# Optimization experiments

Hardware: AMD Instinct MI355X
Metric: run time of the kernel (lower is better)

The kernel has to match this reference:

```python
import math
import jax, jax.numpy as jnp
import numpy as np

B, C_IN, H, W = 2, 64, 256, 512
C_OUT, KH, KW = 64, 3, 3
STRIDE, PAD, DIL = 1, 1, 1


def equi_offsets(pano_H, pano_W, kH, kW, dtype=jnp.float32):
    """Geometry-derived per-pixel offsets for equirectangular deform-conv.
    Returns (off_y, off_x), each [K, pano_H, pano_W], K = kH*kW (row-major)."""
    K = kH * kW
    u = jnp.arange(pano_W, dtype=dtype)
    v = jnp.arange(pano_H, dtype=dtype)
    phi = (u - pano_W / 2.0) / pano_W * (2.0 * math.pi)   # longitude per column
    theta = -(v - pano_H / 2.0) / pano_H * math.pi        # latitude per row
    # R_y(phi): [W,3,3]
    cp, sp = jnp.cos(phi), jnp.sin(phi)
    z, o = jnp.zeros_like(cp), jnp.ones_like(cp)
    Ry = jnp.stack([jnp.stack([cp, z, sp], -1),
                    jnp.stack([z, o, z], -1),
                    jnp.stack([-sp, z, cp], -1)], -2)
    # R_x(theta): [H,3,3]
    ct, st = jnp.cos(theta), jnp.sin(theta)
    zh, oh = jnp.zeros_like(ct), jnp.ones_like(ct)
    Rx = jnp.stack([jnp.stack([oh, zh, zh], -1),
                    jnp.stack([zh, ct, -st], -1),
                    jnp.stack([zh, st, ct], -1)], -2)
    ROT = jnp.einsum('wij,hjk->hwik', Ry, Rx)             # [H,W,3,3]
    # Pinhole rays for the kernel window
    fov_w = kW * (2.0 * math.pi / pano_W)
    focal = (kW / 2.0) / math.tan(fov_w / 2.0)
    hg = (jnp.arange(kH, dtype=dtype)[:, None] + 0.5 - kH / 2.0)
    wg = (jnp.arange(kW, dtype=dtype)[None, :] + 0.5 - kW / 2.0)
    hg = jnp.broadcast_to(hg, (kH, kW)).reshape(K)
    wg = jnp.broadcast_to(wg, (kH, kW)).reshape(K)
    rays0 = jnp.stack([wg / focal, hg / focal, jnp.ones(K, dtype)], 0)  # inv_K @ [w,h,1]
    rays0 = rays0 / jnp.linalg.norm(rays0, axis=0, keepdims=True)
    rays = jnp.einsum('hwik,kn->hwin', ROT, rays0)        # [H,W,3,K]
    phi2 = jnp.arctan2(rays[..., 0, :], rays[..., 2, :])
    th2 = jnp.arcsin(jnp.clip(rays[..., 1, :], -1.0, 1.0))
    x = pano_W / (2.0 * math.pi) * phi2 + pano_W / 2.0    # [H,W,K]
    y = pano_H / math.pi * th2 + pano_H / 2.0
    off_x = x - (wg[None, None, :] + u[None, :, None])
    off_y = y - (hg[None, None, :] + v[:, None, None])
    return jnp.transpose(off_y, (2, 0, 1)), jnp.transpose(off_x, (2, 0, 1))


def deform_conv2d(x, weight, bias, off_y, off_x, stride, pad, dil):
    """Deformable conv (groups=1) with zero-padded bilinear sampling.
    x: [B,C,Hi,Wi]; weight: [O,C,kH,kW]; off_y/off_x: [K,Ho,Wo]."""
    Bn, C, Hi, Wi = x.shape
    O, _, kH, kW = weight.shape
    K, Ho, Wo = off_y.shape
    ky = jnp.broadcast_to(jnp.arange(kH)[:, None], (kH, kW)).reshape(K).astype(x.dtype)
    kx = jnp.broadcast_to(jnp.arange(kW)[None, :], (kH, kW)).reshape(K).astype(x.dtype)
    base_y = jnp.arange(Ho, dtype=x.dtype) * stride - pad
    base_x = jnp.arange(Wo, dtype=x.dtype) * stride - pad
    py = base_y[None, :, None] + ky[:, None, None] * dil + off_y   # [K,Ho,Wo]
    px = base_x[None, None, :] + kx[:, None, None] * dil + off_x
    y0f = jnp.floor(py)
    x0f = jnp.floor(px)
    wy1 = py - y0f
    wx1 = px - x0f
    iy0 = y0f.astype(jnp.int32)
    ix0 = x0f.astype(jnp.int32)
    iy1, ix1 = iy0 + 1, ix0 + 1
    xf = x.reshape(Bn, C, Hi * Wi)

    def corner(iy, ix, w):
        valid = (iy >= 0) & (iy < Hi) & (ix >= 0) & (ix < Wi)
        idx = jnp.clip(iy, 0, Hi - 1) * Wi + jnp.clip(ix, 0, Wi - 1)
        g = xf[:, :, idx]                                  # [B,C,K,Ho,Wo]
        return g * (w * valid.astype(x.dtype))[None, None]

    samp = (corner(iy0, ix0, (1 - wy1) * (1 - wx1))
            + corner(iy0, ix1, (1 - wy1) * wx1)
            + corner(iy1, ix0, wy1 * (1 - wx1))
            + corner(iy1, ix1, wy1 * wx1))                 # [B,C,K,Ho,Wo]
    out = jnp.einsum('bckhw,ock->bohw', samp, weight.reshape(O, C, K))
    return out + bias[None, :, None, None]


def setup_inputs() -> dict:
    key = jax.random.key(0)
    k1, k2, k3 = jax.random.split(key, 3)
    x = jax.random.normal(k1, (B, C_IN, H, W), dtype=jnp.float32)
    fan_in = C_IN * KH * KW
    weight = jax.random.normal(k2, (C_OUT, C_IN, KH, KW), dtype=jnp.float32) / math.sqrt(fan_in)
    bias = jax.random.normal(k3, (C_OUT,), dtype=jnp.float32) * 0.01
    return {"x": x, "weight": weight, "bias": bias}


def reference(x, weight, bias):
    Hi, Wi = x.shape[-2:]
    pano_W = (Wi + 2 * PAD - DIL * (KW - 1) - 1) // STRIDE + 1
    pano_H = (Hi + 2 * PAD - DIL * (KH - 1) - 1) // STRIDE + 1
    off_y, off_x = equi_offsets(pano_H, pano_W, KH, KW, x.dtype)
    return deform_conv2d(x, weight, bias, off_y, off_x, STRIDE, PAD, DIL)
```

## Files before the change

kernel.cpp:

```cpp
#include <hip/hip_runtime.h>
#include <math.h>

namespace {

typedef short  short8 __attribute__((ext_vector_type(8)));
typedef float  f32x4  __attribute__((ext_vector_type(4)));

constexpr int BB = 2, CC = 64, HH = 256, WW = 512, OO = 64, KK = 9;
constexpr int PXB  = 128;
constexpr int NGRP = 32;
constexpr int CHW_F = 6 * WW;
constexpr int BUF_F = 2 * CHW_F;
constexpr int SSTR  = 42;

__device__ __forceinline__ uint rne_bf16(float f) {
  uint u = __float_as_uint(f);
  return (u + 0x7fffu + ((u >> 16) & 1u)) >> 16;
}

__global__ __launch_bounds__(256, 2) void equiconv_mfma(
    const float* __restrict__ x, const float* __restrict__ wgt,
    const float* __restrict__ bias, float* __restrict__ out)
{
  __shared__ __align__(16) float  lbx[2][BUF_F];
  __shared__ __align__(16) ushort Sb[PXB * SSTR];

  const int tid  = threadIdx.x;
  const int wid  = tid >> 6, lane = tid & 63;
  const int p    = tid & (PXB - 1);
  const int cc   = tid >> 7;
  const int w    = blockIdx.x * PXB + p;
  const int h    = blockIdx.y;
  const int b    = blockIdx.z;

  int   jx[KK][4];
  float cw[KK][4];
  {
#pragma clang fp contract(off)
    const float TWO_PI_F = (float)(2.0 * M_PI);
    const float PI_F     = (float)M_PI;
    const float XS       = (float)(512.0 / (2.0 * M_PI));
    const float YS       = (float)(256.0 / M_PI);

    const float uf = (float)w, vf = (float)h;
    const float phi   = ((uf - 256.0f) / 512.0f) * TWO_PI_F;
    const float theta = ((-(vf - 128.0f)) / 256.0f) * PI_F;

    const float sp = (float)sin((double)phi);
    const float cp = (float)cos((double)phi);
    const float st = (float)sin((double)theta);
    const float ct = (float)cos((double)theta);

    const float R00 = cp;        const float R01 = sp * st;  const float R02 = sp * ct;
                    const float R11 = ct;       const float R12 = -st;
    const float R20 = -sp;       const float R21 = cp * st;  const float R22 = cp * ct;

    const double focal_d = 1.5 / tan(0.5 * (3.0 * (2.0 * M_PI / 512.0)));
    const float  focal_f = (float)focal_d;

    for (int k = 0; k < KK; ++k) {
      const float wgk = (float)(k % 3) + 0.5f - 1.5f;
      const float hgk = (float)(k / 3) + 0.5f - 1.5f;

      float rx0 = wgk / focal_f, ry0 = hgk / focal_f, rz0 = 1.0f;
      const float nrm = sqrtf(((rx0 * rx0) + (ry0 * ry0)) + (rz0 * rz0));
      rx0 = rx0 / nrm; ry0 = ry0 / nrm; rz0 = rz0 / nrm;

      const float r0 = ((R00 * rx0) + (R01 * ry0)) + (R02 * rz0);
      const float r1 =               ((R11 * ry0)) + (R12 * rz0);
      const float r2 = ((R20 * rx0) + (R21 * ry0)) + (R22 * rz0);

      const float phi2 = (float)atan2((double)r0, (double)r2);
      float r1c = r1;
      if (r1c >  1.0f) r1c =  1.0f;
      if (r1c < -1.0f) r1c = -1.0f;
      const float th2 = (float)asin((double)r1c);

      const float xx = (XS * phi2) + 256.0f;
      const float yy = (YS * th2)  + 128.0f;

      const float Ax = (float)(w + (k % 3) - 1);
      const float Ay = (float)(h + (k / 3) - 1);
      const float px = Ax + (xx - Ax);
      const float py = Ay + (yy - Ay);

      const float x0f = floorf(px), y0f = floorf(py);
      const float wx1 = px - x0f,   wy1 = py - y0f;
      const int ix0 = (int)x0f, iy0 = (int)y0f;
      const int ix1 = ix0 + 1,  iy1 = iy0 + 1;
      const bool vx0 = (ix0 >= 0) && (ix0 < WW);
      const bool vx1 = (ix1 >= 0) && (ix1 < WW);
      const bool vy0 = (iy0 >= 0) && (iy0 < HH);
      const bool vy1 = (iy1 >= 0) && (iy1 < HH);
      const int cx0 = min(max(ix0, 0), WW - 1);
      const int cx1 = min(max(ix1, 0), WW - 1);
      const int cy0 = min(max(iy0, 0), HH - 1);
      const int cy1 = min(max(iy1, 0), HH - 1);
      const int j0 = cy0 - h + 2;
      const int j1 = cy1 - h + 2;
      jx[k][0] = j0 * WW + cx0;
      jx[k][1] = j0 * WW + cx1;
      jx[k][2] = j1 * WW + cx0;
      jx[k][3] = j1 * WW + cx1;
      const float wy0f = 1.0f - wy1, wx0f = 1.0f - wx1;
      cw[k][0] = (wy0f * wx0f) * ((vy0 && vx0) ? 1.0f : 0.0f);
      cw[k][1] = (wy0f * wx1)  * ((vy0 && vx1) ? 1.0f : 0.0f);
      cw[k][2] = (wy1 * wx0f)  * ((vy1 && vx0) ? 1.0f : 0.0f);
      cw[k][3] = (wy1 * wx1)   * ((vy1 && vx1) ? 1.0f : 0.0f);
    }
  }

  {
    uint* S32 = (uint*)Sb;
#pragma unroll
    for (int i = 0; i < 11; ++i) {
      const int idx = tid + 256 * i;
      if (idx < (PXB * SSTR) / 2) S32[idx] = 0u;
    }
  }

  auto stage = [&](int bi, int g2) {
#pragma unroll
    for (int i = 0; i < 6; ++i) {
      const int ci  = wid * 6 + i;
      const int ccs = ci / 12, r2 = ci % 12, j = r2 >> 1, half = r2 & 1;
      const int srow = min(max(h - 2 + j, 0), HH - 1);
      const int ch   = g2 * 2 + ccs;
      const float* src = x + (((size_t)b * CC + ch) * HH + srow) * WW + half * 256 + lane * 4;
      __builtin_amdgcn_global_load_lds(
          (const __attribute__((address_space(1))) void*)src,
          (__attribute__((address_space(3))) void*)&lbx[bi][ccs * CHW_F + j * 512 + half * 256],
          16, 0, 0);
    }
  };

  f32x4 acc[4][2];
#pragma unroll
  for (int ot = 0; ot < 4; ++ot)
#pragma unroll
    for (int pt = 0; pt < 2; ++pt) acc[ot][pt] = (f32x4){0.f, 0.f, 0.f, 0.f};

  stage(0, 0);

#pragma unroll 1
  for (int g = 0; g < NGRP; ++g) {
    const int bi = g & 1;

    short8 A[4];
    {
      const int lg = lane >> 4;
      const int c  = g * 2 + (lg >> 1);
#pragma unroll
      for (int ot = 0; ot < 4; ++ot) {
        const int o = ot * 16 + (lane & 15);
        const float* wp9 = wgt + ((size_t)o * 64 + c) * 9;
        short8 a;
        if ((lg & 1) == 0) {
#pragma unroll
          for (int j = 0; j < 8; ++j) a[j] = (short)(ushort)rne_bf16(wp9[j]);
        } else {
          a = (short8){0, 0, 0, 0, 0, 0, 0, 0};
          a[0] = (short)(ushort)rne_bf16(wp9[8]);
        }
        A[ot] = a;
      }
    }

    if (g < NGRP - 1) {
      stage(bi ^ 1, g + 1);
      asm volatile("s_waitcnt vmcnt(6)" ::: "memory");
    } else {
      asm volatile("s_waitcnt vmcnt(0)" ::: "memory");
    }
    __builtin_amdgcn_sched_barrier(0);
    __builtin_amdgcn_s_barrier();
    __builtin_amdgcn_sched_barrier(0);

    {
      const float* Lc = &lbx[bi][cc * CHW_F];
      float s[KK];
#pragma unroll
      for (int k = 0; k < KK; ++k) {
        s[k] = fmaf(cw[k][3], Lc[jx[k][3]],
               fmaf(cw[k][2], Lc[jx[k][2]],
               fmaf(cw[k][1], Lc[jx[k][1]],
                    cw[k][0] * Lc[jx[k][0]])));
      }
      const uint b0 = rne_bf16(s[0]), b1 = rne_bf16(s[1]), b2 = rne_bf16(s[2]);
      const uint b3 = rne_bf16(s[3]), b4 = rne_bf16(s[4]), b5 = rne_bf16(s[5]);
      const uint b6 = rne_bf16(s[6]), b7 = rne_bf16(s[7]), b8 = rne_bf16(s[8]);
      uint2* Sr = (uint2*)(Sb + p * SSTR + cc * 16);
      Sr[0] = make_uint2(b0 | (b1 << 16), b2 | (b3 << 16));
      Sr[1] = make_uint2(b4 | (b5 << 16), b6 | (b7 << 16));
      Sb[p * SSTR + cc * 16 + 8] = (ushort)b8;
    }

    asm volatile("s_waitcnt lgkmcnt(0)" ::: "memory");
    __builtin_amdgcn_sched_barrier(0);
    __builtin_amdgcn_s_barrier();
    __builtin_amdgcn_sched_barrier(0);

    short8 Bfr[2];
#pragma unroll
    for (int pt = 0; pt < 2; ++pt) {
      const int prow = wid * 32 + pt * 16 + (lane & 15);
      Bfr[pt] = *(const short8*)(Sb + prow * SSTR + ((lane >> 4) & 3) * 8);
    }
    asm volatile("s_waitcnt lgkmcnt(0)" ::: "memory");
    __builtin_amdgcn_sched_barrier(0);
#pragma unroll
    for (int ot = 0; ot < 4; ++ot)
#pragma unroll
      for (int pt = 0; pt < 2; ++pt)
        acc[ot][pt] = __builtin_amdgcn_mfma_f32_16x16x32_bf16(A[ot], Bfr[pt], acc[ot][pt], 0, 0, 0);
    __builtin_amdgcn_sched_barrier(0);
  }

#pragma unroll
  for (int ot = 0; ot < 4; ++ot) {
    const int o = ot * 16 + ((lane >> 4) & 3) * 4;
#pragma unroll
    for (int pt = 0; pt < 2; ++pt) {
      const int wcol = blockIdx.x * PXB + wid * 32 + pt * 16 + (lane & 15);
#pragma unroll
      for (int r = 0; r < 4; ++r)
        out[(((size_t)b * OO + (o + r)) * HH + h) * WW + wcol] = acc[ot][pt][r] + bias[o + r];
    }
  }
}

}

extern "C" void kernel_launch(void* const* d_in, const int* in_sizes, int n_in,
                              void* d_out, int out_size, void* d_ws, size_t ws_size,
                              hipStream_t stream) {
  const float* x      = (const float*)d_in[0];
  const float* weight = (const float*)d_in[1];
  const float* bias   = (const float*)d_in[2];
  float* out          = (float*)d_out;

  dim3 grid(WW / PXB, HH, BB);
  hipLaunchKernelGGL(equiconv_mfma, grid, dim3(256), 0, stream,
                     x, weight, bias, out);
}
```

Measured before the change: 388.5 us.

## Process two output rows per block and prepack bf16 weights in workspace

Each block now covers two adjacent output rows with 512 threads. It stages a 7-row input window per channel pair that both rows share, instead of each row loading its own 6-row window. A small pre-kernel converts the weights into MFMA-fragment-ordered bf16 in the workspace, so the main loop does one vector load instead of per-lane fp32 gathers and rounding. The costs are roughly double the LDS per block, which may hurt occupancy despite the 512,4 launch bound, and an extra kernel launch.

```diff
diff --git a/kernel.cpp b/kernel.cpp
--- a/kernel.cpp
+++ b/kernel.cpp
@@ -9,8 +9,7 @@
 constexpr int BB = 2, CC = 64, HH = 256, WW = 512, OO = 64, KK = 9;
 constexpr int PXB  = 128;
 constexpr int NGRP = 32;
-constexpr int CHW_F = 6 * WW;
-constexpr int BUF_F = 2 * CHW_F;
+constexpr int CHW_F = 7 * WW;
 constexpr int SSTR  = 42;
 
 __device__ __forceinline__ uint rne_bf16(float f) {
@@ -18,19 +17,33 @@
   return (u + 0x7fffu + ((u >> 16) & 1u)) >> 16;
 }
 
-__global__ __launch_bounds__(256, 2) void equiconv_mfma(
+__global__ void wpack_kernel(const float* __restrict__ wgt, ushort* __restrict__ wp) {
+  int e = blockIdx.x * 256 + threadIdx.x;
+  int j = e & 7, lane = (e >> 3) & 63, ot = (e >> 9) & 3, g = e >> 11;
+  int o  = ot * 16 + (lane & 15);
+  int kp = g * 32 + ((lane >> 4) & 3) * 8 + j;
+  int c = kp >> 4, kk = kp & 15;
+  float v = (kk < 9) ? wgt[(o * 64 + c) * 9 + kk] : 0.0f;
+  wp[e] = (ushort)rne_bf16(v);
+}
+
+__global__ __launch_bounds__(512, 4) void equiconv_mfma(
     const float* __restrict__ x, const float* __restrict__ wgt,
-    const float* __restrict__ bias, float* __restrict__ out)
+    const float* __restrict__ bias, float* __restrict__ out,
+    const ushort* __restrict__ wp)
 {
-  __shared__ __align__(16) float  lbx[2][BUF_F];
-  __shared__ __align__(16) ushort Sb[PXB * SSTR];
+  __shared__ __align__(16) float  lbx[2][2 * CHW_F];
+  __shared__ __align__(16) ushort Sb[256 * SSTR];
 
   const int tid  = threadIdx.x;
   const int wid  = tid >> 6, lane = tid & 63;
-  const int p    = tid & (PXB - 1);
-  const int cc   = tid >> 7;
+  const int q    = tid & 255;
+  const int r    = q >> 7;
+  const int p    = q & 127;
+  const int cc   = tid >> 8;
   const int w    = blockIdx.x * PXB + p;
-  const int h    = blockIdx.y;
+  const int h0   = blockIdx.y * 2;
+  const int h    = h0 + r;
   const int b    = blockIdx.z;
 
   int   jx[KK][4];
@@ -96,8 +109,8 @@
       const int cx1 = min(max(ix1, 0), WW - 1);
       const int cy0 = min(max(iy0, 0), HH - 1);
       const int cy1 = min(max(iy1, 0), HH - 1);
-      const int j0 = cy0 - h + 2;
-      const int j1 = cy1 - h + 2;
+      const int j0 = cy0 - h0 + 2;
+      const int j1 = cy1 - h0 + 2;
       jx[k][0] = j0 * WW + cx0;
       jx[k][1] = j0 * WW + cx1;
       jx[k][2] = j1 * WW + cx0;
@@ -114,22 +127,23 @@
     uint* S32 = (uint*)Sb;
 #pragma unroll
     for (int i = 0; i < 11; ++i) {
-      const int idx = tid + 256 * i;
-      if (idx < (PXB * SSTR) / 2) S32[idx] = 0u;
+      const int idx = tid + 512 * i;
+      if (idx < (256 * SSTR) / 2) S32[idx] = 0u;
     }
   }
 
   auto stage = [&](int bi, int g2) {
 #pragma unroll
-    for (int i = 0; i < 6; ++i) {
-      const int ci  = wid * 6 + i;
-      const int ccs = ci / 12, r2 = ci % 12, j = r2 >> 1, half = r2 & 1;
-      const int srow = min(max(h - 2 + j, 0), HH - 1);
-      const int ch   = g2 * 2 + ccs;
-      const float* src = x + (((size_t)b * CC + ch) * HH + srow) * WW + half * 256 + lane * 4;
+    for (int i = 0; i < 4; ++i) {
+      const int ci  = wid * 4 + i;
+      const int cci = (ci < 28) ? ci : (ci - 28);
+      const int ch  = cci / 14, rem = cci % 14, j = rem >> 1, half = rem & 1;
+      const int srow = min(max(h0 - 2 + j, 0), HH - 1);
+      const int chan = g2 * 2 + ch;
+      const float* src = x + (((size_t)b * CC + chan) * HH + srow) * WW + half * 256 + lane * 4;
       __builtin_amdgcn_global_load_lds(
           (const __attribute__((address_space(1))) void*)src,
-          (__attribute__((address_space(3))) void*)&lbx[bi][ccs * CHW_F + j * 512 + half * 256],
+          (__attribute__((address_space(3))) void*)&lbx[bi][ch * CHW_F + j * 512 + half * 256],
           16, 0, 0);
     }
   };
@@ -147,7 +161,11 @@
     const int bi = g & 1;
 
     short8 A[4];
-    {
+    if (wp) {
+#pragma unroll
+      for (int ot = 0; ot < 4; ++ot)
+        A[ot] = *(const short8*)(wp + ((size_t)(g * 4 + ot) * 64 + lane) * 8);
+    } else {
       const int lg = lane >> 4;
       const int c  = g * 2 + (lg >> 1);
 #pragma unroll
@@ -165,10 +183,11 @@
         A[ot] = a;
       }
     }
+    __builtin_amdgcn_sched_barrier(0);
 
     if (g < NGRP - 1) {
       stage(bi ^ 1, g + 1);
-      asm volatile("s_waitcnt vmcnt(6)" ::: "memory");
+      asm volatile("s_waitcnt vmcnt(4)" ::: "memory");
     } else {
       asm volatile("s_waitcnt vmcnt(0)" ::: "memory");
     }
@@ -189,10 +208,10 @@
       const uint b0 = rne_bf16(s[0]), b1 = rne_bf16(s[1]), b2 = rne_bf16(s[2]);
       const uint b3 = rne_bf16(s[3]), b4 = rne_bf16(s[4]), b5 = rne_bf16(s[5]);
       const uint b6 = rne_bf16(s[6]), b7 = rne_bf16(s[7]), b8 = rne_bf16(s[8]);
-      uint2* Sr = (uint2*)(Sb + p * SSTR + cc * 16);
+      uint2* Sr = (uint2*)(Sb + q * SSTR + cc * 16);
       Sr[0] = make_uint2(b0 | (b1 << 16), b2 | (b3 << 16));
       Sr[1] = make_uint2(b4 | (b5 << 16), b6 | (b7 << 16));
-      Sb[p * SSTR + cc * 16 + 8] = (ushort)b8;
+      Sb[q * SSTR + cc * 16 + 8] = (ushort)b8;
     }
 
     asm volatile("s_waitcnt lgkmcnt(0)" ::: "memory");
@@ -218,13 +237,15 @@
 
 #pragma unroll
   for (int ot = 0; ot < 4; ++ot) {
-    const int o = ot * 16 + ((lane >> 4) & 3) * 4;
+    const int ob = ot * 16 + ((lane >> 4) & 3) * 4;
 #pragma unroll
     for (int pt = 0; pt < 2; ++pt) {
-      const int wcol = blockIdx.x * PXB + wid * 32 + pt * 16 + (lane & 15);
-#pragma unroll
-      for (int r = 0; r < 4; ++r)
-        out[(((size_t)b * OO + (o + r)) * HH + h) * WW + wcol] = acc[ot][pt][r] + bias[o + r];
+      const int wq   = wid * 32 + pt * 16 + (lane & 15);
+      const int rowo = h0 + (wq >> 7);
+      const int colo = blockIdx.x * PXB + (wq & 127);
+#pragma unroll
+      for (int rr = 0; rr < 4; ++rr)
+        out[(((size_t)b * OO + (ob + rr)) * HH + rowo) * WW + colo] = acc[ot][pt][rr] + bias[ob + rr];
     }
   }
 }
@@ -239,7 +260,12 @@
   const float* bias   = (const float*)d_in[2];
   float* out          = (float*)d_out;
 
-  dim3 grid(WW / PXB, HH, BB);
-  hipLaunchKernelGGL(equiconv_mfma, grid, dim3(256), 0, stream,
-                     x, weight, bias, out);
-}
+  const bool use_ws = (d_ws != nullptr && ws_size >= 131072);
+  ushort* wp = use_ws ? (ushort*)d_ws : nullptr;
+  if (use_ws)
+    hipLaunchKernelGGL(wpack_kernel, dim3(256), dim3(256), 0, stream, weight, wp);
+
+  dim3 grid(WW / PXB, HH / 2, BB);
+  hipLaunchKernelGGL(equiconv_mfma, grid, dim3(512), 0, stream,
+                     x, weight, bias, out, (const ushort*)wp);
+}
```

After: 672.8 us. +73.2%, slower.
